# Performance work log

Hardware: AMD Instinct MI355X
Metric: run time of the kernel (lower is better)

The kernel has to match this reference:

```python
import jax, jax.numpy as jnp
import numpy as np

LOG_CLAMP = -100.0  # torch BCELoss clamps log terms at -100

def setup_inputs() -> dict:
    key = jax.random.key(0)
    k1, k2 = jax.random.split(key)
    N = 16777216
    x = jax.random.uniform(k1, (N,), dtype=jnp.float32)
    gt = jax.random.randint(k2, (N,), 0, 2, dtype=jnp.int32)
    return {"x": x, "gt": gt}

def reference(x, gt):
    x = x.reshape(-1)
    gtf = gt.reshape(-1).astype(x.dtype)
    n = jnp.asarray(gtf.shape[0], x.dtype)
    s = gtf.sum()  # number of positives
    pa = n * n / (n - s) / 2.0 / s
    weight_0 = pa * s / n          # weight for gt == 0
    weight_1 = pa * (n - s) / n    # weight for gt == 1
    weight = jnp.where(gtf == 0, weight_0, weight_1)
    log_x = jnp.maximum(jnp.log(x), LOG_CLAMP)
    log_1mx = jnp.maximum(jnp.log1p(-x), LOG_CLAMP)
    bce = -(gtf * log_x + (1.0 - gtf) * log_1mx)
    return jnp.mean(weight * bce)
```

## Files before the change

### kernel.cpp

```cpp
#include <hip/hip_runtime.h>

#define LOG2_CLAMP -144.269504088896f
#define LN2 0.69314718055994530942
#define GRID 2048
#define BLOCK 256


__device__ __forceinline__ float log2_clamped(float v) {
  return fmaxf(__builtin_amdgcn_logf(v), LOG2_CLAMP);
}

#define ACC1(xe, ge)                              \
  {                                               \
    float t = (ge) ? (xe) : 1.0f - (xe);          \
    float l = log2_clamped(t);                    \
    tot -= l;                                     \
    s1 -= (ge) ? l : 0.0f;                        \
    icnt += (ge) ? 1 : 0;                         \
  }

#define ACC4(xv, gv)                              \
  ACC1(xv.x, gv.x) ACC1(xv.y, gv.y)               \
  ACC1(xv.z, gv.z) ACC1(xv.w, gv.w)

__global__ __launch_bounds__(BLOCK) void bce_stage1(
    const float* __restrict__ x, const int* __restrict__ gt,
    int n, float* __restrict__ part) {
  float tot = 0.0f, s1 = 0.0f;
  int icnt = 0;

  const int tid = blockIdx.x * BLOCK + threadIdx.x;
  const int stride = GRID * BLOCK;
  const int n4 = n >> 2;
  const float4* __restrict__ x4 = reinterpret_cast<const float4*>(x);
  const int4* __restrict__ g4 = reinterpret_cast<const int4*>(gt);

  int i = tid;
  for (; i + 7 * stride < n4; i += 8 * stride) {
    float4 xa = x4[i];
    float4 xb = x4[i + stride];
    float4 xc = x4[i + 2 * stride];
    float4 xd = x4[i + 3 * stride];
    float4 xe = x4[i + 4 * stride];
    float4 xf = x4[i + 5 * stride];
    float4 xg = x4[i + 6 * stride];
    float4 xh = x4[i + 7 * stride];
    int4 ga = g4[i];
    int4 gb = g4[i + stride];
    int4 gc = g4[i + 2 * stride];
    int4 gd = g4[i + 3 * stride];
    int4 ge = g4[i + 4 * stride];
    int4 gf = g4[i + 5 * stride];
    int4 gg = g4[i + 6 * stride];
    int4 gh = g4[i + 7 * stride];
    ACC4(xa, ga) ACC4(xb, gb) ACC4(xc, gc) ACC4(xd, gd)
    ACC4(xe, ge) ACC4(xf, gf) ACC4(xg, gg) ACC4(xh, gh)
  }
  for (; i < n4; i += stride) {
    float4 xa = x4[i];
    int4 ga = g4[i];
    ACC4(xa, ga)
  }
  for (int j = (n4 << 2) + tid; j < n; j += stride) {
    float xv = x[j];
    int gv = gt[j];
    ACC1(xv, gv)
  }

  float cnt = (float)icnt;

  for (int off = 32; off > 0; off >>= 1) {
    tot += __shfl_down(tot, off, 64);
    s1  += __shfl_down(s1, off, 64);
    cnt += __shfl_down(cnt, off, 64);
  }

  __shared__ float red[3][BLOCK / 64];
  const int lane = threadIdx.x & 63;
  const int wave = threadIdx.x >> 6;
  if (lane == 0) {
    red[0][wave] = tot;
    red[1][wave] = s1;
    red[2][wave] = cnt;
  }
  __syncthreads();
  if (threadIdx.x == 0) {
    part[blockIdx.x]            = red[0][0] + red[0][1] + red[0][2] + red[0][3];
    part[GRID + blockIdx.x]     = red[1][0] + red[1][1] + red[1][2] + red[1][3];
    part[2 * GRID + blockIdx.x] = red[2][0] + red[2][1] + red[2][2] + red[2][3];
  }
}

__global__ __launch_bounds__(BLOCK) void bce_stage2(
    const float* __restrict__ part, float* __restrict__ out, double n) {
  double tot = 0.0, s1 = 0.0, cnt = 0.0;
  for (int i = threadIdx.x; i < GRID; i += BLOCK) {
    tot += (double)part[i];
    s1  += (double)part[GRID + i];
    cnt += (double)part[2 * GRID + i];
  }
  for (int off = 32; off > 0; off >>= 1) {
    tot += __shfl_down(tot, off, 64);
    s1  += __shfl_down(s1, off, 64);
    cnt += __shfl_down(cnt, off, 64);
  }
  __shared__ double red[3][BLOCK / 64];
  const int lane = threadIdx.x & 63;
  const int wave = threadIdx.x >> 6;
  if (lane == 0) {
    red[0][wave] = tot;
    red[1][wave] = s1;
    red[2][wave] = cnt;
  }
  __syncthreads();
  if (threadIdx.x == 0) {
    double T = (red[0][0] + red[0][1] + red[0][2] + red[0][3]) * LN2;
    double S1 = (red[1][0] + red[1][1] + red[1][2] + red[1][3]) * LN2;
    double s = red[2][0] + red[2][1] + red[2][2] + red[2][3];
    double S0 = T - S1;
    out[0] = (float)(S1 / (2.0 * s) + S0 / (2.0 * (n - s)));
  }
}

extern "C" void kernel_launch(void* const* d_in, const int* in_sizes, int n_in,
                              void* d_out, int out_size, void* d_ws, size_t ws_size,
                              hipStream_t stream) {
  const float* x = (const float*)d_in[0];
  const int* gt = (const int*)d_in[1];
  float* out = (float*)d_out;
  int n = in_sizes[0];

  float* part = (float*)d_ws;

  bce_stage1<<<GRID, BLOCK, 0, stream>>>(x, gt, n, part);
  bce_stage2<<<1, BLOCK, 0, stream>>>(part, out, (double)n);
}
```

Measured before the change: 149.4 us.

## Use contiguous per-block chunks with nontemporal double-buffered loads

Each block now walks one contiguous chunk of the input instead of a grid-strided layout. Loads use nontemporal builtins with a two-deep software prefetch in registers, replacing the 8-way unrolled batch of loads. The goal is better DRAM locality and less cache pollution for a streaming reduction. The trade-off is fewer loads in flight per thread than the 8-way unroll, which could lower achieved memory bandwidth.

New measurement: 140.5 us. 6.0% less time.

```diff
diff --git a/kernel.cpp b/kernel.cpp
--- a/kernel.cpp
+++ b/kernel.cpp
@@ -4,6 +4,9 @@
 #define LN2 0.69314718055994530942
 #define GRID 2048
 #define BLOCK 256
+
+typedef float fx4 __attribute__((ext_vector_type(4)));
+typedef int ix4 __attribute__((ext_vector_type(4)));
 
 
 __device__ __forceinline__ float log2_clamped(float v) {
@@ -29,39 +32,39 @@
   float tot = 0.0f, s1 = 0.0f;
   int icnt = 0;
 
-  const int tid = blockIdx.x * BLOCK + threadIdx.x;
-  const int stride = GRID * BLOCK;
   const int n4 = n >> 2;
-  const float4* __restrict__ x4 = reinterpret_cast<const float4*>(x);
-  const int4* __restrict__ g4 = reinterpret_cast<const int4*>(gt);
+  const int chunk = (n4 + GRID - 1) / GRID;
+  const int start = blockIdx.x * chunk;
+  const int end = min(start + chunk, n4);
+  const fx4* __restrict__ x4 = reinterpret_cast<const fx4*>(x);
+  const ix4* __restrict__ g4 = reinterpret_cast<const ix4*>(gt);
 
-  int i = tid;
-  for (; i + 7 * stride < n4; i += 8 * stride) {
-    float4 xa = x4[i];
-    float4 xb = x4[i + stride];
-    float4 xc = x4[i + 2 * stride];
-    float4 xd = x4[i + 3 * stride];
-    float4 xe = x4[i + 4 * stride];
-    float4 xf = x4[i + 5 * stride];
-    float4 xg = x4[i + 6 * stride];
-    float4 xh = x4[i + 7 * stride];
-    int4 ga = g4[i];
-    int4 gb = g4[i + stride];
-    int4 gc = g4[i + 2 * stride];
-    int4 gd = g4[i + 3 * stride];
-    int4 ge = g4[i + 4 * stride];
-    int4 gf = g4[i + 5 * stride];
-    int4 gg = g4[i + 6 * stride];
-    int4 gh = g4[i + 7 * stride];
-    ACC4(xa, ga) ACC4(xb, gb) ACC4(xc, gc) ACC4(xd, gd)
-    ACC4(xe, ge) ACC4(xf, gf) ACC4(xg, gg) ACC4(xh, gh)
+  int i = start + (int)threadIdx.x;
+  fx4 xcur = {0.5f, 0.5f, 0.5f, 0.5f}, xnext = {0.5f, 0.5f, 0.5f, 0.5f};
+  ix4 gcur = {0, 0, 0, 0}, gnext = {0, 0, 0, 0};
+  if (i < end) {
+    xcur = __builtin_nontemporal_load(&x4[i]);
+    gcur = __builtin_nontemporal_load(&g4[i]);
   }
-  for (; i < n4; i += stride) {
-    float4 xa = x4[i];
-    int4 ga = g4[i];
-    ACC4(xa, ga)
+  if (i + BLOCK < end) {
+    xnext = __builtin_nontemporal_load(&x4[i + BLOCK]);
+    gnext = __builtin_nontemporal_load(&g4[i + BLOCK]);
   }
-  for (int j = (n4 << 2) + tid; j < n; j += stride) {
+  for (; i < end; i += BLOCK) {
+    fx4 xc = xcur;
+    ix4 gc = gcur;
+    xcur = xnext;
+    gcur = gnext;
+    const int ip2 = i + 2 * BLOCK;
+    if (ip2 < end) {
+      xnext = __builtin_nontemporal_load(&x4[ip2]);
+      gnext = __builtin_nontemporal_load(&g4[ip2]);
+    }
+    ACC4(xc, gc)
+  }
+
+  for (int j = (n4 << 2) + blockIdx.x * BLOCK + (int)threadIdx.x; j < n;
+       j += GRID * BLOCK) {
     float xv = x[j];
     int gv = gt[j];
     ACC1(xv, gv)
@@ -114,9 +117,9 @@
   }
   __syncthreads();
   if (threadIdx.x == 0) {
-    double T = (red[0][0] + red[0][1] + red[0][2] + red[0][3]) * LN2;
+    double T  = (red[0][0] + red[0][1] + red[0][2] + red[0][3]) * LN2;
     double S1 = (red[1][0] + red[1][1] + red[1][2] + red[1][3]) * LN2;
-    double s = red[2][0] + red[2][1] + red[2][2] + red[2][3];
+    double s  = red[2][0] + red[2][1] + red[2][2] + red[2][3];
     double S0 = T - S1;
     out[0] = (float)(S1 / (2.0 * s) + S0 / (2.0 * (n - s)));
   }
```
